# Performance work log

Measured on AMD Instinct MI355X. Metric: run time of the kernel, lower is better.

## Reference

```python
import jax, jax.numpy as jnp
import numpy as np


def setup_inputs() -> dict:
    key = jax.random.key(0)
    k1, k2 = jax.random.split(key)
    B, C, H, W = 32, 512, 32, 32
    NUM_ITEM = 2048
    x = jax.random.normal(k1, (B, C, H, W), dtype=jnp.float32)
    # original uses uniform(-stdv, stdv) with stdv = 1/sqrt(dim)
    stdv = 1.0 / np.sqrt(C)
    mempool = jax.random.uniform(k2, (NUM_ITEM, C), dtype=jnp.float32, minval=-stdv, maxval=stdv)
    return {"x": x, "mempool": mempool, "k": 8}


def reference(x, mempool, k):
    B, C, H, W = x.shape
    num_item = mempool.shape[0]
    # permute to channels-last and flatten spatial: [N, C]
    q = jnp.transpose(x, (0, 2, 3, 1)).reshape(-1, C)
    # gating scores: [N, num_item]
    att = q @ mempool.T
    vals, idx = jax.lax.top_k(att, k)            # [N, k]
    vals = jax.nn.softmax(vals, axis=1)
    # scatter top-k softmax weights into mostly-zero [N, num_item] matrix
    rows = jnp.arange(q.shape[0])[:, None]
    att_sparse = jnp.zeros_like(att).at[rows, idx].set(vals)
    # dense combine: [N, C]
    out = att_sparse @ mempool
    out = out.reshape(B, H, W, C)
    return jnp.transpose(out, (0, 3, 1, 2))
```

## Files before the change

kernel.cpp:

```cpp
#include <hip/hip_runtime.h>

typedef __attribute__((ext_vector_type(4))) float f32x4;
typedef __attribute__((ext_vector_type(8))) short short8;

#define C_    512
#define HW_   1024
#define M_    2048
#define TN    32
#define NTILE 8
#define NKC   16
#define NSTEP (NTILE * NKC)
#define NCAND 16
#define NEG_INF (-1e30f)

#define ATT_BASE   32768
#define ATT_STRIDE 264
#define ARENA_SIZE 49664
#define CV_BASE  32768
#define CI_BASE  36992
#define SEL_BASE 41216
#define RFV_BASE 43264
#define QS 260

__device__ __forceinline__ unsigned short f2bf(float f) {
    unsigned u = __builtin_bit_cast(unsigned, f);
    u += 0x7fffu + ((u >> 16) & 1u);
    return (unsigned short)(u >> 16);
}
__device__ __forceinline__ float bf2f(unsigned short s) {
    return __builtin_bit_cast(float, (unsigned)s << 16);
}

__global__ __launch_bounds__(256) void convk(const float* __restrict__ in,
                                             unsigned short* __restrict__ ob) {
    int gid = blockIdx.x * 256 + threadIdx.x;
    int m  = gid >> 6;
    int ug = gid & 63;
    const float4* p = (const float4*)(in + (size_t)m * C_ + ug * 8);
    float4 v0 = p[0], v1 = p[1];
    int4 o;
    o.x = (int)f2bf(v0.x) | ((int)f2bf(v0.y) << 16);
    o.y = (int)f2bf(v0.z) | ((int)f2bf(v0.w) << 16);
    o.z = (int)f2bf(v1.x) | ((int)f2bf(v1.y) << 16);
    o.w = (int)f2bf(v1.z) | ((int)f2bf(v1.w) << 16);
    int kc = ug >> 2, u = ug & 3;
    *(int4*)((char*)ob + (size_t)kc * 131072 + m * 64 + (u << 4)) = o;
}

__global__ __launch_bounds__(256, 3) void memk(const float* __restrict__ x,
                                               const float* __restrict__ mempool,
                                               const unsigned short* __restrict__ membR,
                                               float* __restrict__ out) {
    __shared__ __align__(16) char arena[ARENA_SIZE];
    unsigned short* att16 = (unsigned short*)(arena + ATT_BASE);
    float* candv  = (float*)(arena + CV_BASE);
    int*   candi  = (int*)(arena + CI_BASE);
    int*   selidx = (int*)(arena + SEL_BASE);
    float* refv   = (float*)(arena + RFV_BASE);
    float* qs     = (float*)arena;
    float* w_lds  = (float*)(arena + 8192);
    int*   i_lds  = (int*)(arena + 9216);

    const int t   = threadIdx.x;
    const int l   = t & 63;
    const int w   = t >> 6;
    const int hi  = l >> 4;
    const int l15 = l & 15;
    const int n0  = blockIdx.x * TN;
    const int b   = n0 >> 10;
    const int hw0 = n0 & 1023;
    const float* xb = x + (size_t)b * C_ * HW_ + hw0;

    {
        const int row = t & 31, g = t >> 5;
        const float* xp = xb + row;
        char* Arow = arena + row * 1024;
        const int swz = (row & 7) << 4;
#pragma unroll 8
        for (int j = 0; j < 32; ++j) {
            int c = g * 64 + 2 * j;
            float f0 = xp[(size_t)c * HW_];
            float f1 = xp[(size_t)(c + 1) * HW_];
            unsigned pk = (unsigned)f2bf(f0) | ((unsigned)f2bf(f1) << 16);
            *(unsigned*)(Arow + ((2 * c) ^ swz)) = pk;
        }
    }
    __syncthreads();

    const int srow = t >> 2, stq = t & 3;
    float sv[8]; int si[8];
#pragma unroll
    for (int p = 0; p < 8; ++p) { sv[p] = NEG_INF; si[p] = 0x7fffffff; }

    const int aswz = (l15 & 7) << 4;
    const char* Ab0 = arena + l15 * 1024;
    const char* Ab1 = arena + (16 + l15) * 1024;
    const int hio = hi << 4;
    const char* bbase = (const char*)membR + w * 4096 + l15 * 64 + hi * 16;

    short8 bq[4], bp[4];
    {
        const char* p0 = bbase;
        const char* p1 = bbase + 131072;
#pragma unroll
        for (int itf = 0; itf < 4; ++itf) {
            bq[itf] = *(const short8*)(p0 + itf * 1024);
            bp[itf] = *(const short8*)(p1 + itf * 1024);
        }
    }

    for (int tile = 0; tile < NTILE; ++tile) {
        f32x4 acc[2][4];
#pragma unroll
        for (int rf = 0; rf < 2; ++rf)
#pragma unroll
            for (int itf = 0; itf < 4; ++itf) acc[rf][itf] = (f32x4)0.f;

#pragma unroll 4
        for (int kc = 0; kc < NKC; ++kc) {
            int s = tile * NKC + kc + 2;
            int sc = (s < NSTEP) ? s : 0;
            const char* pn = bbase + (size_t)(sc & 15) * 131072 + (size_t)(sc >> 4) * 16384;
            short8 bn[4];
#pragma unroll
            for (int itf = 0; itf < 4; ++itf) bn[itf] = *(const short8*)(pn + itf * 1024);

            const int ao = (kc * 64 + hio) ^ aswz;
            short8 a0 = *(const short8*)(Ab0 + ao);
            short8 a1 = *(const short8*)(Ab1 + ao);
#pragma unroll
            for (int itf = 0; itf < 4; ++itf) {
                acc[0][itf] = __builtin_amdgcn_mfma_f32_16x16x32_bf16(a0, bq[itf], acc[0][itf], 0, 0, 0);
                acc[1][itf] = __builtin_amdgcn_mfma_f32_16x16x32_bf16(a1, bq[itf], acc[1][itf], 0, 0, 0);
            }
#pragma unroll
            for (int itf = 0; itf < 4; ++itf) { bq[itf] = bp[itf]; bp[itf] = bn[itf]; }
        }

#pragma unroll
        for (int rf = 0; rf < 2; ++rf)
#pragma unroll
            for (int itf = 0; itf < 4; ++itf) {
                int col = w * 64 + itf * 16 + l15;
#pragma unroll
                for (int reg = 0; reg < 4; ++reg)
                    att16[(rf * 16 + hi * 4 + reg) * ATT_STRIDE + col] = f2bf(acc[rf][itf][reg]);
            }
        __syncthreads();

        const int m0 = tile * 256;
        if (t < 128) {
            const unsigned short* arow = att16 + srow * ATT_STRIDE;
#pragma unroll
            for (int v = 0; v < 8; ++v) {
                short8 pv = *(const short8*)(arow + stq * 8 + v * 32);
                float f[8];
#pragma unroll
                for (int e = 0; e < 8; ++e) f[e] = bf2f((unsigned short)pv[e]);
                float m01 = fmaxf(f[0], f[1]), m23 = fmaxf(f[2], f[3]);
                float m45 = fmaxf(f[4], f[5]), m67 = fmaxf(f[6], f[7]);
                float vmax = fmaxf(fmaxf(m01, m23), fmaxf(m45, m67));
                if (vmax > sv[0]) {
#pragma unroll
                    for (int e = 0; e < 8; ++e) {
                        if (f[e] > sv[0]) {
                            sv[0] = f[e]; si[0] = m0 + stq * 8 + v * 32 + e;
#pragma unroll
                            for (int p = 0; p < 7; ++p) {
                                if (sv[p] > sv[p + 1]) {
                                    float tv = sv[p]; sv[p] = sv[p + 1]; sv[p + 1] = tv;
                                    int   ti = si[p]; si[p] = si[p + 1]; si[p + 1] = ti;
                                }
                            }
                        }
                    }
                }
            }
        }
        __syncthreads();
    }

    if (t < 128) {
#pragma unroll
        for (int p = 0; p < 8; ++p) {
            candv[srow * 33 + stq * 8 + p] = sv[p];
            candi[srow * 33 + stq * 8 + p] = si[p];
        }
    }
    __syncthreads();

    if (t < TN) {
        const int row = t;
        int pos[4] = {7, 7, 7, 7};
        for (int s = 0; s < NCAND; ++s) {
            float vb = NEG_INF; int ib = 0x7fffffff; int qb = 0;
#pragma unroll
            for (int q = 0; q < 4; ++q) {
                if (pos[q] >= 0) {
                    float v = candv[row * 33 + q * 8 + pos[q]];
                    int  ii = candi[row * 33 + q * 8 + pos[q]];
                    if (v > vb || (v == vb && ii < ib)) { vb = v; ib = ii; qb = q; }
                }
            }
            selidx[row * NCAND + s] = ib;
#pragma unroll
            for (int q = 0; q < 4; ++q) if (q == qb) --pos[q];
        }
    }
    __syncthreads();

    int cnd[2];
    cnd[0] = selidx[t];
    cnd[1] = selidx[t + 256];
    float racc[2] = {0.f, 0.f};
#pragma unroll
    for (int ch = 0; ch < 2; ++ch) {
        const int c0 = ch * 256;
        __syncthreads();
        {
            const int r = t & 31, g = t >> 5;
            const float* xp = xb + r;
#pragma unroll 2
            for (int j = 0; j < 8; ++j) {
                int c = g * 32 + j * 4;
                f32x4 v;
                v[0] = xp[(size_t)(c0 + c + 0) * HW_];
                v[1] = xp[(size_t)(c0 + c + 1) * HW_];
                v[2] = xp[(size_t)(c0 + c + 2) * HW_];
                v[3] = xp[(size_t)(c0 + c + 3) * HW_];
                *(f32x4*)&qs[r * QS + c] = v;
            }
        }
        __syncthreads();
#pragma unroll
        for (int pp = 0; pp < 2; ++pp) {
            const int row = (t + 256 * pp) >> 4;
            const float4* mp = (const float4*)(mempool + (size_t)cnd[pp] * C_ + c0);
            const f32x4* qrow = (const f32x4*)&qs[row * QS];
            float a = racc[pp];
#pragma unroll 8
            for (int u = 0; u < 64; ++u) {
                f32x4 q4 = qrow[u];
                float4 m4 = mp[u];
                a = fmaf(q4[0], m4.x, a);
                a = fmaf(q4[1], m4.y, a);
                a = fmaf(q4[2], m4.z, a);
                a = fmaf(q4[3], m4.w, a);
            }
            racc[pp] = a;
        }
    }
    refv[t] = racc[0];
    refv[t + 256] = racc[1];
    __syncthreads();

    if (t < TN) {
        const int row = t;
        float rv[16]; int ri[16];
#pragma unroll
        for (int s = 0; s < 16; ++s) { rv[s] = refv[row * 16 + s]; ri[s] = selidx[row * 16 + s]; }
        float wv8[8]; int wi8[8];
#pragma unroll
        for (int sel = 0; sel < 8; ++sel) {
            float vb = NEG_INF; int ib = 0x7fffffff; int sb = 0;
            for (int s = 0; s < 16; ++s) {
                if (rv[s] > vb || (rv[s] == vb && ri[s] < ib)) { vb = rv[s]; ib = ri[s]; sb = s; }
            }
            rv[sb] = NEG_INF;
            wv8[sel] = vb; wi8[sel] = ib;
        }
        const float mx = wv8[0];
        float e[8]; float sum = 0.f;
#pragma unroll
        for (int j = 0; j < 8; ++j) { e[j] = expf(wv8[j] - mx); sum += e[j]; }
        const float inv = 1.f / sum;
#pragma unroll
        for (int j = 0; j < 8; ++j) { w_lds[row * 8 + j] = e[j] * inv; i_lds[row * 8 + j] = wi8[j]; }
    }
    __syncthreads();

    const int crow = t & 31;
    const int cw   = t >> 5;
    float wreg[8]; int ireg[8];
#pragma unroll
    for (int j = 0; j < 8; ++j) { wreg[j] = w_lds[crow * 8 + j]; ireg[j] = i_lds[crow * 8 + j]; }
    float* outb = out + (size_t)b * C_ * HW_ + hw0 + crow;
#pragma unroll 2
    for (int cg = 0; cg < 16; ++cg) {
        const int c = cw * 64 + cg * 4;
        float o0 = 0.f, o1 = 0.f, o2 = 0.f, o3 = 0.f;
#pragma unroll
        for (int j = 0; j < 8; ++j) {
            const float4 mp4 = *(const float4*)&mempool[(size_t)ireg[j] * C_ + c];
            o0 = fmaf(wreg[j], mp4.x, o0);
            o1 = fmaf(wreg[j], mp4.y, o1);
            o2 = fmaf(wreg[j], mp4.z, o2);
            o3 = fmaf(wreg[j], mp4.w, o3);
        }
        outb[(size_t)(c + 0) * HW_] = o0;
        outb[(size_t)(c + 1) * HW_] = o1;
        outb[(size_t)(c + 2) * HW_] = o2;
        outb[(size_t)(c + 3) * HW_] = o3;
    }
}

extern "C" void kernel_launch(void* const* d_in, const int* in_sizes, int n_in,
                              void* d_out, int out_size, void* d_ws, size_t ws_size,
                              hipStream_t stream) {
    const float* x       = (const float*)d_in[0];
    const float* mempool = (const float*)d_in[1];
    unsigned short* membR = (unsigned short*)d_ws;
    float* o = (float*)d_out;
    convk<<<dim3(512), dim3(256), 0, stream>>>(mempool, membR);
    memk<<<dim3(1024), dim3(256), 0, stream>>>(x, mempool, membR, o);
}
```

Before: 444.0 us.

## Double-buffer score tiles to overlap top-k scan with MFMA and prefetch refinement

Scores are now staged in two alternating LDS buffers, so the top-k scan of the previous tile runs alongside the next tile's GEMM. This removes one barrier per tile. The B-operand register prefetch is deepened from two steps to three, and the second x channel-half load for the fp32 refinement is issued before the first half's dot products. The cost is a larger LDS arena and occupancy lowered from 3 to 2 blocks per CU, plus more live registers.

```diff
diff --git a/kernel.cpp b/kernel.cpp
--- a/kernel.cpp
+++ b/kernel.cpp
@@ -9,17 +9,19 @@
 #define TN    32
 #define NTILE 8
 #define NKC   16
-#define NSTEP (NTILE * NKC)
 #define NCAND 16
 #define NEG_INF (-1e30f)
 
-#define ATT_BASE   32768
 #define ATT_STRIDE 264
-#define ARENA_SIZE 49664
+#define BUF0 32768
+#define BUF1 49664
+#define ARENA_SIZE 66560
 #define CV_BASE  32768
 #define CI_BASE  36992
 #define SEL_BASE 41216
 #define RFV_BASE 43264
+#define WL_BASE  45312
+#define IL_BASE  46336
 #define QS 260
 
 __device__ __forceinline__ unsigned short f2bf(float f) {
@@ -47,19 +49,49 @@
     *(int4*)((char*)ob + (size_t)kc * 131072 + m * 64 + (u << 4)) = o;
 }
 
-__global__ __launch_bounds__(256, 3) void memk(const float* __restrict__ x,
+__device__ __forceinline__ void scan_tile(const unsigned short* arow, int m0,
+                                          float* sv, int* si, int stq) {
+#pragma unroll
+    for (int v = 0; v < 8; ++v) {
+        short8 pv = *(const short8*)(arow + stq * 8 + v * 32);
+        float f[8];
+#pragma unroll
+        for (int e = 0; e < 8; ++e) f[e] = bf2f((unsigned short)pv[e]);
+        float m01 = fmaxf(f[0], f[1]), m23 = fmaxf(f[2], f[3]);
+        float m45 = fmaxf(f[4], f[5]), m67 = fmaxf(f[6], f[7]);
+        float vmax = fmaxf(fmaxf(m01, m23), fmaxf(m45, m67));
+        if (vmax > sv[0]) {
+#pragma unroll
+            for (int e = 0; e < 8; ++e) {
+                if (f[e] > sv[0]) {
+                    sv[0] = f[e]; si[0] = m0 + stq * 8 + v * 32 + e;
+#pragma unroll
+                    for (int p = 0; p < 7; ++p) {
+                        if (sv[p] > sv[p + 1]) {
+                            float tv = sv[p]; sv[p] = sv[p + 1]; sv[p + 1] = tv;
+                            int   ti = si[p]; si[p] = si[p + 1]; si[p + 1] = ti;
+                        }
+                    }
+                }
+            }
+        }
+    }
+}
+
+__global__ __launch_bounds__(256, 2) void memk(const float* __restrict__ x,
                                                const float* __restrict__ mempool,
                                                const unsigned short* __restrict__ membR,
                                                float* __restrict__ out) {
     __shared__ __align__(16) char arena[ARENA_SIZE];
-    unsigned short* att16 = (unsigned short*)(arena + ATT_BASE);
+    unsigned short* att0 = (unsigned short*)(arena + BUF0);
+    unsigned short* att1 = (unsigned short*)(arena + BUF1);
     float* candv  = (float*)(arena + CV_BASE);
     int*   candi  = (int*)(arena + CI_BASE);
     int*   selidx = (int*)(arena + SEL_BASE);
     float* refv   = (float*)(arena + RFV_BASE);
     float* qs     = (float*)arena;
-    float* w_lds  = (float*)(arena + 8192);
-    int*   i_lds  = (int*)(arena + 9216);
+    float* w_lds  = (float*)(arena + WL_BASE);
+    int*   i_lds  = (int*)(arena + IL_BASE);
 
     const int t   = threadIdx.x;
     const int l   = t & 63;
@@ -98,18 +130,18 @@
     const int hio = hi << 4;
     const char* bbase = (const char*)membR + w * 4096 + l15 * 64 + hi * 16;
 
-    short8 bq[4], bp[4];
-    {
-        const char* p0 = bbase;
-        const char* p1 = bbase + 131072;
-#pragma unroll
-        for (int itf = 0; itf < 4; ++itf) {
-            bq[itf] = *(const short8*)(p0 + itf * 1024);
-            bp[itf] = *(const short8*)(p1 + itf * 1024);
-        }
+    short8 bq[4], b1[4], b2[4];
+#pragma unroll
+    for (int itf = 0; itf < 4; ++itf) {
+        bq[itf] = *(const short8*)(bbase + itf * 1024);
+        b1[itf] = *(const short8*)(bbase + 131072 + itf * 1024);
+        b2[itf] = *(const short8*)(bbase + 262144 + itf * 1024);
     }
 
     for (int tile = 0; tile < NTILE; ++tile) {
+        unsigned short* dumpBuf = (tile & 1) ? att1 : att0;
+        unsigned short* scanBuf = (tile & 1) ? att0 : att1;
+
         f32x4 acc[2][4];
 #pragma unroll
         for (int rf = 0; rf < 2; ++rf)
@@ -118,9 +150,9 @@
 
 #pragma unroll 4
         for (int kc = 0; kc < NKC; ++kc) {
-            int s = tile * NKC + kc + 2;
-            int sc = (s < NSTEP) ? s : 0;
-            const char* pn = bbase + (size_t)(sc & 15) * 131072 + (size_t)(sc >> 4) * 16384;
+            int s3 = tile * NKC + kc + 3;
+            if (s3 > 127) s3 = 127;
+            const char* pn = bbase + (size_t)(s3 & 15) * 131072 + (size_t)(s3 >> 4) * 16384;
             short8 bn[4];
 #pragma unroll
             for (int itf = 0; itf < 4; ++itf) bn[itf] = *(const short8*)(pn + itf * 1024);
@@ -134,7 +166,7 @@
                 acc[1][itf] = __builtin_amdgcn_mfma_f32_16x16x32_bf16(a1, bq[itf], acc[1][itf], 0, 0, 0);
             }
 #pragma unroll
-            for (int itf = 0; itf < 4; ++itf) { bq[itf] = bp[itf]; bp[itf] = bn[itf]; }
+            for (int itf = 0; itf < 4; ++itf) { bq[itf] = b1[itf]; b1[itf] = b2[itf]; b2[itf] = bn[itf]; }
         }
 
 #pragma unroll
@@ -144,41 +176,16 @@
                 int col = w * 64 + itf * 16 + l15;
 #pragma unroll
                 for (int reg = 0; reg < 4; ++reg)
-                    att16[(rf * 16 + hi * 4 + reg) * ATT_STRIDE + col] = f2bf(acc[rf][itf][reg]);
-            }
+                    dumpBuf[(rf * 16 + hi * 4 + reg) * ATT_STRIDE + col] = f2bf(acc[rf][itf][reg]);
+            }
+
+        if (tile > 0 && t < 128)
+            scan_tile(scanBuf + srow * ATT_STRIDE, (tile - 1) * 256, sv, si, stq);
+
         __syncthreads();
-
-        const int m0 = tile * 256;
-        if (t < 128) {
-            const unsigned short* arow = att16 + srow * ATT_STRIDE;
-#pragma unroll
-            for (int v = 0; v < 8; ++v) {
-                short8 pv = *(const short8*)(arow + stq * 8 + v * 32);
-                float f[8];
-#pragma unroll
-                for (int e = 0; e < 8; ++e) f[e] = bf2f((unsigned short)pv[e]);
-                float m01 = fmaxf(f[0], f[1]), m23 = fmaxf(f[2], f[3]);
-                float m45 = fmaxf(f[4], f[5]), m67 = fmaxf(f[6], f[7]);
-                float vmax = fmaxf(fmaxf(m01, m23), fmaxf(m45, m67));
-                if (vmax > sv[0]) {
-#pragma unroll
-                    for (int e = 0; e < 8; ++e) {
-                        if (f[e] > sv[0]) {
-                            sv[0] = f[e]; si[0] = m0 + stq * 8 + v * 32 + e;
-#pragma unroll
-                            for (int p = 0; p < 7; ++p) {
-                                if (sv[p] > sv[p + 1]) {
-                                    float tv = sv[p]; sv[p] = sv[p + 1]; sv[p + 1] = tv;
-                                    int   ti = si[p]; si[p] = si[p + 1]; si[p + 1] = ti;
-                                }
-                            }
-                        }
-                    }
-                }
-            }
-        }
-        __syncthreads();
-    }
+    }
+    if (t < 128)
+        scan_tile(att1 + srow * ATT_STRIDE, 7 * 256, sv, si, stq);
 
     if (t < 128) {
 #pragma unroll
@@ -213,42 +220,68 @@
     cnd[0] = selidx[t];
     cnd[1] = selidx[t + 256];
     float racc[2] = {0.f, 0.f};
-#pragma unroll
-    for (int ch = 0; ch < 2; ++ch) {
-        const int c0 = ch * 256;
-        __syncthreads();
-        {
-            const int r = t & 31, g = t >> 5;
-            const float* xp = xb + r;
+    const int qr = t & 31, qg = t >> 5;
+    const float* xq = xb + qr;
+
+    f32x4 r0[8];
 #pragma unroll 2
-            for (int j = 0; j < 8; ++j) {
-                int c = g * 32 + j * 4;
-                f32x4 v;
-                v[0] = xp[(size_t)(c0 + c + 0) * HW_];
-                v[1] = xp[(size_t)(c0 + c + 1) * HW_];
-                v[2] = xp[(size_t)(c0 + c + 2) * HW_];
-                v[3] = xp[(size_t)(c0 + c + 3) * HW_];
-                *(f32x4*)&qs[r * QS + c] = v;
-            }
-        }
-        __syncthreads();
-#pragma unroll
-        for (int pp = 0; pp < 2; ++pp) {
-            const int row = (t + 256 * pp) >> 4;
-            const float4* mp = (const float4*)(mempool + (size_t)cnd[pp] * C_ + c0);
-            const f32x4* qrow = (const f32x4*)&qs[row * QS];
-            float a = racc[pp];
+    for (int j = 0; j < 8; ++j) {
+        int c = qg * 32 + j * 4;
+        r0[j][0] = xq[(size_t)(c + 0) * HW_];
+        r0[j][1] = xq[(size_t)(c + 1) * HW_];
+        r0[j][2] = xq[(size_t)(c + 2) * HW_];
+        r0[j][3] = xq[(size_t)(c + 3) * HW_];
+    }
+#pragma unroll
+    for (int j = 0; j < 8; ++j) *(f32x4*)&qs[qr * QS + qg * 32 + j * 4] = r0[j];
+    __syncthreads();
+
+    f32x4 r1[8];
+#pragma unroll 2
+    for (int j = 0; j < 8; ++j) {
+        int c = 256 + qg * 32 + j * 4;
+        r1[j][0] = xq[(size_t)(c + 0) * HW_];
+        r1[j][1] = xq[(size_t)(c + 1) * HW_];
+        r1[j][2] = xq[(size_t)(c + 2) * HW_];
+        r1[j][3] = xq[(size_t)(c + 3) * HW_];
+    }
+#pragma unroll
+    for (int pp = 0; pp < 2; ++pp) {
+        const int row = (t + 256 * pp) >> 4;
+        const float4* mp = (const float4*)(mempool + (size_t)cnd[pp] * C_);
+        const f32x4* qrow = (const f32x4*)&qs[row * QS];
+        float a = racc[pp];
 #pragma unroll 8
-            for (int u = 0; u < 64; ++u) {
-                f32x4 q4 = qrow[u];
-                float4 m4 = mp[u];
-                a = fmaf(q4[0], m4.x, a);
-                a = fmaf(q4[1], m4.y, a);
-                a = fmaf(q4[2], m4.z, a);
-                a = fmaf(q4[3], m4.w, a);
-            }
-            racc[pp] = a;
-        }
+        for (int u = 0; u < 64; ++u) {
+            f32x4 q4 = qrow[u];
+            float4 m4 = mp[u];
+            a = fmaf(q4[0], m4.x, a);
+            a = fmaf(q4[1], m4.y, a);
+            a = fmaf(q4[2], m4.z, a);
+            a = fmaf(q4[3], m4.w, a);
+        }
+        racc[pp] = a;
+    }
+    __syncthreads();
+#pragma unroll
+    for (int j = 0; j < 8; ++j) *(f32x4*)&qs[qr * QS + qg * 32 + j * 4] = r1[j];
+    __syncthreads();
+#pragma unroll
+    for (int pp = 0; pp < 2; ++pp) {
+        const int row = (t + 256 * pp) >> 4;
+        const float4* mp = (const float4*)(mempool + (size_t)cnd[pp] * C_ + 256);
+        const f32x4* qrow = (const f32x4*)&qs[row * QS];
+        float a = racc[pp];
+#pragma unroll 8
+        for (int u = 0; u < 64; ++u) {
+            f32x4 q4 = qrow[u];
+            float4 m4 = mp[u];
+            a = fmaf(q4[0], m4.x, a);
+            a = fmaf(q4[1], m4.y, a);
+            a = fmaf(q4[2], m4.z, a);
+            a = fmaf(q4[3], m4.w, a);
+        }
+        racc[pp] = a;
     }
     refv[t] = racc[0];
     refv[t + 256] = racc[1];
```

Measured after the change: 462.6 us. 1.04x slower.

## Split fused kernel into tiled GEMM with per-tile top-8 and separate merge kernel

Applied to the files above, without the earlier changes.

Replaces the monolithic per-32-row kernel with a 2D-tiled GEMM kernel (128 rows x 128 items per block) that streams double-buffered bf16 activations through LDS, computes per-tile top-8 candidates, and writes packed value/index words to workspace. A second kernel merges the 16 per-tile candidate lists, then keeps the existing fp32 rescoring, softmax and combine. The aim is better B-operand reuse and parallelism across item tiles for the GEMM. The cost is an extra launch, a global round-trip for candidates, and repeated conversion of x across the 16 column tiles.

```diff
diff --git a/kernel.cpp b/kernel.cpp
--- a/kernel.cpp
+++ b/kernel.cpp
@@ -6,21 +6,7 @@
 #define C_    512
 #define HW_   1024
 #define M_    2048
-#define TN    32
-#define NTILE 8
-#define NKC   16
-#define NSTEP (NTILE * NKC)
-#define NCAND 16
 #define NEG_INF (-1e30f)
-
-#define ATT_BASE   32768
-#define ATT_STRIDE 264
-#define ARENA_SIZE 49664
-#define CV_BASE  32768
-#define CI_BASE  36992
-#define SEL_BASE 41216
-#define RFV_BASE 43264
-#define QS 260
 
 __device__ __forceinline__ unsigned short f2bf(float f) {
     unsigned u = __builtin_bit_cast(unsigned, f);
@@ -29,6 +15,20 @@
 }
 __device__ __forceinline__ float bf2f(unsigned short s) {
     return __builtin_bit_cast(float, (unsigned)s << 16);
+}
+__device__ __forceinline__ float pkval(unsigned u) {
+    return __builtin_bit_cast(float, u & 0xFFFF0000u);
+}
+
+__device__ __forceinline__ void insert8(float v, int idx, float* sv, int* si) {
+    sv[0] = v; si[0] = idx;
+#pragma unroll
+    for (int p = 0; p < 7; ++p) {
+        if (sv[p] > sv[p + 1]) {
+            float tv = sv[p]; sv[p] = sv[p + 1]; sv[p + 1] = tv;
+            int   ti = si[p]; si[p] = si[p + 1]; si[p + 1] = ti;
+        }
+    }
 }
 
 __global__ __launch_bounds__(256) void convk(const float* __restrict__ in,
@@ -47,140 +47,198 @@
     *(int4*)((char*)ob + (size_t)kc * 131072 + m * 64 + (u << 4)) = o;
 }
 
-__global__ __launch_bounds__(256, 3) void memk(const float* __restrict__ x,
-                                               const float* __restrict__ mempool,
-                                               const unsigned short* __restrict__ membR,
-                                               float* __restrict__ out) {
-    __shared__ __align__(16) char arena[ARENA_SIZE];
-    unsigned short* att16 = (unsigned short*)(arena + ATT_BASE);
-    float* candv  = (float*)(arena + CV_BASE);
-    int*   candi  = (int*)(arena + CI_BASE);
-    int*   selidx = (int*)(arena + SEL_BASE);
-    float* refv   = (float*)(arena + RFV_BASE);
-    float* qs     = (float*)arena;
-    float* w_lds  = (float*)(arena + 8192);
-    int*   i_lds  = (int*)(arena + 9216);
+#define K2_ABUF  9216
+#define K2_CAND  33792
+#define K2_ARENA 41984
+
+__global__ __launch_bounds__(256, 2) void gemmk(const float* __restrict__ x,
+                                                const unsigned short* __restrict__ membR,
+                                                unsigned int* __restrict__ gcand) {
+    __shared__ __align__(16) char arena[K2_ARENA];
+    unsigned short* att16 = (unsigned short*)arena;
+    unsigned int*   candt = (unsigned int*)(arena + K2_CAND);
 
     const int t   = threadIdx.x;
     const int l   = t & 63;
     const int w   = t >> 6;
     const int hi  = l >> 4;
     const int l15 = l & 15;
-    const int n0  = blockIdx.x * TN;
+    const int colTile = blockIdx.x;
+    const int rowTile = blockIdx.y;
+    const int n0  = rowTile * 128;
     const int b   = n0 >> 10;
     const int hw0 = n0 & 1023;
     const float* xb = x + (size_t)b * C_ * HW_ + hw0;
 
+    const char* bbase = (const char*)membR + colTile * 8192 + l15 * 64 + hi * 16;
+
+    short8 bq[8], bn[8];
+#pragma unroll
+    for (int itf = 0; itf < 8; ++itf) bq[itf] = *(const short8*)(bbase + itf * 1024);
+
     {
-        const int row = t & 31, g = t >> 5;
-        const float* xp = xb + row;
-        char* Arow = arena + row * 1024;
-        const int swz = (row & 7) << 4;
-#pragma unroll 8
-        for (int j = 0; j < 32; ++j) {
-            int c = g * 64 + 2 * j;
-            float f0 = xp[(size_t)c * HW_];
-            float f1 = xp[(size_t)(c + 1) * HW_];
-            unsigned pk = (unsigned)f2bf(f0) | ((unsigned)f2bf(f1) << 16);
-            *(unsigned*)(Arow + ((2 * c) ^ swz)) = pk;
-        }
-    }
-    __syncthreads();
+        char* buf = arena;
+#pragma unroll
+        for (int cc = 0; cc < 8; cc += 2) {
+            int c = w * 8 + cc;
+#pragma unroll
+            for (int rr = 0; rr < 2; ++rr) {
+                int row = rr * 64 + l;
+                float f0 = xb[(size_t)c * HW_ + row];
+                float f1 = xb[(size_t)(c + 1) * HW_ + row];
+                unsigned pk = (unsigned)f2bf(f0) | ((unsigned)f2bf(f1) << 16);
+                *(unsigned*)(buf + row * 72 + c * 2) = pk;
+            }
+        }
+    }
+    __syncthreads();
+
+    f32x4 acc[2][8];
+#pragma unroll
+    for (int rf = 0; rf < 2; ++rf)
+#pragma unroll
+        for (int itf = 0; itf < 8; ++itf) acc[rf][itf] = (f32x4)0.f;
+
+#pragma unroll 2
+    for (int kc = 0; kc < 16; ++kc) {
+        if (kc < 15) {
+            char* buf = arena + ((kc + 1) & 1) * K2_ABUF;
+            const float* xc = xb + (size_t)(kc + 1) * 32 * HW_;
+#pragma unroll
+            for (int cc = 0; cc < 8; cc += 2) {
+                int c = w * 8 + cc;
+#pragma unroll
+                for (int rr = 0; rr < 2; ++rr) {
+                    int row = rr * 64 + l;
+                    float f0 = xc[(size_t)c * HW_ + row];
+                    float f1 = xc[(size_t)(c + 1) * HW_ + row];
+                    unsigned pk = (unsigned)f2bf(f0) | ((unsigned)f2bf(f1) << 16);
+                    *(unsigned*)(buf + row * 72 + c * 2) = pk;
+                }
+            }
+        }
+        {
+            int s = (kc + 1 < 16) ? kc + 1 : 15;
+            const char* pn = bbase + (size_t)s * 131072;
+#pragma unroll
+            for (int itf = 0; itf < 8; ++itf) bn[itf] = *(const short8*)(pn + itf * 1024);
+        }
+        const char* cur = arena + (kc & 1) * K2_ABUF;
+        short8 a0 = *(const short8*)(cur + (w * 32 + l15) * 72 + hi * 16);
+        short8 a1 = *(const short8*)(cur + (w * 32 + 16 + l15) * 72 + hi * 16);
+#pragma unroll
+        for (int itf = 0; itf < 8; ++itf) {
+            acc[0][itf] = __builtin_amdgcn_mfma_f32_16x16x32_bf16(a0, bq[itf], acc[0][itf], 0, 0, 0);
+            acc[1][itf] = __builtin_amdgcn_mfma_f32_16x16x32_bf16(a1, bq[itf], acc[1][itf], 0, 0, 0);
+        }
+#pragma unroll
+        for (int itf = 0; itf < 8; ++itf) bq[itf] = bn[itf];
+        __syncthreads();
+    }
+
+#pragma unroll
+    for (int rf = 0; rf < 2; ++rf)
+#pragma unroll
+        for (int itf = 0; itf < 8; ++itf) {
+            int col = itf * 16 + l15;
+#pragma unroll
+            for (int reg = 0; reg < 4; ++reg) {
+                int row = w * 32 + rf * 16 + hi * 4 + reg;
+                att16[row * 132 + col] = f2bf(acc[rf][itf][reg]);
+            }
+        }
+    __syncthreads();
+
+    const int sr = t >> 1, hf = t & 1;
+    float sv[8]; int si[8];
+#pragma unroll
+    for (int p = 0; p < 8; ++p) { sv[p] = NEG_INF; si[p] = 0x7fffffff; }
+    {
+        const unsigned short* arow = att16 + sr * 132 + hf * 64;
+#pragma unroll
+        for (int v = 0; v < 8; ++v) {
+            short8 pv = *(const short8*)(arow + v * 8);
+            float f[8];
+#pragma unroll
+            for (int e = 0; e < 8; ++e) f[e] = bf2f((unsigned short)pv[e]);
+            float m01 = fmaxf(f[0], f[1]), m23 = fmaxf(f[2], f[3]);
+            float m45 = fmaxf(f[4], f[5]), m67 = fmaxf(f[6], f[7]);
+            float vmax = fmaxf(fmaxf(m01, m23), fmaxf(m45, m67));
+            if (vmax > sv[0]) {
+#pragma unroll
+                for (int e = 0; e < 8; ++e)
+                    if (f[e] > sv[0]) insert8(f[e], hf * 64 + v * 8 + e, sv, si);
+            }
+        }
+    }
+    __syncthreads();
+#pragma unroll
+    for (int p = 0; p < 8; ++p)
+        candt[(sr * 2 + hf) * 8 + p] =
+            (__builtin_bit_cast(unsigned, sv[p]) & 0xFFFF0000u) |
+            (unsigned)(colTile * 128 + si[p]);
+    __syncthreads();
+
+    if (t < 128) {
+        const unsigned* c0 = candt + (t * 2 + 0) * 8;
+        const unsigned* c1 = candt + (t * 2 + 1) * 8;
+        int p0 = 7, p1 = 7;
+        unsigned res[8];
+#pragma unroll
+        for (int s = 0; s < 8; ++s) {
+            unsigned u0 = c0[p0 < 0 ? 0 : p0], u1 = c1[p1 < 0 ? 0 : p1];
+            float v0 = (p0 >= 0) ? pkval(u0) : NEG_INF;
+            float v1 = (p1 >= 0) ? pkval(u1) : NEG_INF;
+            bool take0 = (v0 > v1) || (v0 == v1 && (int)(u0 & 0xFFFFu) < (int)(u1 & 0xFFFFu));
+            if (p1 < 0) take0 = true;
+            if (p0 < 0) take0 = false;
+            if (take0) { res[s] = u0; --p0; } else { res[s] = u1; --p1; }
+        }
+        unsigned int* gp = gcand + (size_t)(n0 + t) * 128 + colTile * 8;
+        *(uint4*)gp       = make_uint4(res[0], res[1], res[2], res[3]);
+        *(uint4*)(gp + 4) = make_uint4(res[4], res[5], res[6], res[7]);
+    }
+}
+
+#define QS 260
+#define K3_SEL 33280
+#define K3_RFV 35328
+#define K3_WL  37376
+#define K3_IL  38400
+#define K3_ARENA 39424
+#define NCAND 16
+
+__global__ __launch_bounds__(256, 4) void mergek(const float* __restrict__ x,
+                                                 const float* __restrict__ mempool,
+                                                 const unsigned int* __restrict__ gcand,
+                                                 float* __restrict__ out) {
+    __shared__ __align__(16) char arena[K3_ARENA];
+    float* candv  = (float*)arena;
+    int*   candi  = (int*)(arena + 4224);
+    float* qs     = (float*)arena;
+    int*   selidx = (int*)(arena + K3_SEL);
+    float* refv   = (float*)(arena + K3_RFV);
+    float* w_lds  = (float*)(arena + K3_WL);
+    int*   i_lds  = (int*)(arena + K3_IL);
+
+    const int t   = threadIdx.x;
+    const int n0  = blockIdx.x * 32;
+    const int b   = n0 >> 10;
+    const int hw0 = n0 & 1023;
+    const float* xb = x + (size_t)b * C_ * HW_ + hw0;
 
     const int srow = t >> 2, stq = t & 3;
     float sv[8]; int si[8];
 #pragma unroll
     for (int p = 0; p < 8; ++p) { sv[p] = NEG_INF; si[p] = 0x7fffffff; }
-
-    const int aswz = (l15 & 7) << 4;
-    const char* Ab0 = arena + l15 * 1024;
-    const char* Ab1 = arena + (16 + l15) * 1024;
-    const int hio = hi << 4;
-    const char* bbase = (const char*)membR + w * 4096 + l15 * 64 + hi * 16;
-
-    short8 bq[4], bp[4];
-    {
-        const char* p0 = bbase;
-        const char* p1 = bbase + 131072;
-#pragma unroll
-        for (int itf = 0; itf < 4; ++itf) {
-            bq[itf] = *(const short8*)(p0 + itf * 1024);
-            bp[itf] = *(const short8*)(p1 + itf * 1024);
-        }
-    }
-
-    for (int tile = 0; tile < NTILE; ++tile) {
-        f32x4 acc[2][4];
-#pragma unroll
-        for (int rf = 0; rf < 2; ++rf)
-#pragma unroll
-            for (int itf = 0; itf < 4; ++itf) acc[rf][itf] = (f32x4)0.f;
-
+    if (t < 128) {
+        const unsigned int* gc = gcand + (size_t)(n0 + srow) * 128 + stq * 32;
 #pragma unroll 4
-        for (int kc = 0; kc < NKC; ++kc) {
-            int s = tile * NKC + kc + 2;
-            int sc = (s < NSTEP) ? s : 0;
-            const char* pn = bbase + (size_t)(sc & 15) * 131072 + (size_t)(sc >> 4) * 16384;
-            short8 bn[4];
-#pragma unroll
-            for (int itf = 0; itf < 4; ++itf) bn[itf] = *(const short8*)(pn + itf * 1024);
-
-            const int ao = (kc * 64 + hio) ^ aswz;
-            short8 a0 = *(const short8*)(Ab0 + ao);
-            short8 a1 = *(const short8*)(Ab1 + ao);
-#pragma unroll
-            for (int itf = 0; itf < 4; ++itf) {
-                acc[0][itf] = __builtin_amdgcn_mfma_f32_16x16x32_bf16(a0, bq[itf], acc[0][itf], 0, 0, 0);
-                acc[1][itf] = __builtin_amdgcn_mfma_f32_16x16x32_bf16(a1, bq[itf], acc[1][itf], 0, 0, 0);
-            }
-#pragma unroll
-            for (int itf = 0; itf < 4; ++itf) { bq[itf] = bp[itf]; bp[itf] = bn[itf]; }
-        }
-
-#pragma unroll
-        for (int rf = 0; rf < 2; ++rf)
-#pragma unroll
-            for (int itf = 0; itf < 4; ++itf) {
-                int col = w * 64 + itf * 16 + l15;
-#pragma unroll
-                for (int reg = 0; reg < 4; ++reg)
-                    att16[(rf * 16 + hi * 4 + reg) * ATT_STRIDE + col] = f2bf(acc[rf][itf][reg]);
-            }
-        __syncthreads();
-
-        const int m0 = tile * 256;
-        if (t < 128) {
-            const unsigned short* arow = att16 + srow * ATT_STRIDE;
-#pragma unroll
-            for (int v = 0; v < 8; ++v) {
-                short8 pv = *(const short8*)(arow + stq * 8 + v * 32);
-                float f[8];
-#pragma unroll
-                for (int e = 0; e < 8; ++e) f[e] = bf2f((unsigned short)pv[e]);
-                float m01 = fmaxf(f[0], f[1]), m23 = fmaxf(f[2], f[3]);
-                float m45 = fmaxf(f[4], f[5]), m67 = fmaxf(f[6], f[7]);
-                float vmax = fmaxf(fmaxf(m01, m23), fmaxf(m45, m67));
-                if (vmax > sv[0]) {
-#pragma unroll
-                    for (int e = 0; e < 8; ++e) {
-                        if (f[e] > sv[0]) {
-                            sv[0] = f[e]; si[0] = m0 + stq * 8 + v * 32 + e;
-#pragma unroll
-                            for (int p = 0; p < 7; ++p) {
-                                if (sv[p] > sv[p + 1]) {
-                                    float tv = sv[p]; sv[p] = sv[p + 1]; sv[p + 1] = tv;
-                                    int   ti = si[p]; si[p] = si[p + 1]; si[p + 1] = ti;
-                                }
-                            }
-                        }
-                    }
-                }
-            }
-        }
-        __syncthreads();
-    }
-
-    if (t < 128) {
+        for (int j = 0; j < 32; ++j) {
+            unsigned u = gc[j];
+            float v = pkval(u);
+            if (v > sv[0]) insert8(v, (int)(u & 0xFFFFu), sv, si);
+        }
 #pragma unroll
         for (int p = 0; p < 8; ++p) {
             candv[srow * 33 + stq * 8 + p] = sv[p];
@@ -189,7 +247,7 @@
     }
     __syncthreads();
 
-    if (t < TN) {
+    if (t < 32) {
         const int row = t;
         int pos[4] = {7, 7, 7, 7};
         for (int s = 0; s < NCAND; ++s) {
@@ -218,17 +276,17 @@
         const int c0 = ch * 256;
         __syncthreads();
         {
-            const int r = t & 31, g = t >> 5;
-            const float* xp = xb + r;
+            const int qr = t & 31, qg = t >> 5;
+            const float* xp = xb + qr;
 #pragma unroll 2
             for (int j = 0; j < 8; ++j) {
-                int c = g * 32 + j * 4;
+                int c = qg * 32 + j * 4;
                 f32x4 v;
                 v[0] = xp[(size_t)(c0 + c + 0) * HW_];
                 v[1] = xp[(size_t)(c0 + c + 1) * HW_];
                 v[2] = xp[(size_t)(c0 + c + 2) * HW_];
                 v[3] = xp[(size_t)(c0 + c + 3) * HW_];
-                *(f32x4*)&qs[r * QS + c] = v;
+                *(f32x4*)&qs[qr * QS + c] = v;
             }
         }
         __syncthreads();
@@ -254,7 +312,7 @@
     refv[t + 256] = racc[1];
     __syncthreads();
 
-    if (t < TN) {
+    if (t < 32) {
         const int row = t;
         float rv[16]; int ri[16];
 #pragma unroll
@@ -310,7 +368,9 @@
     const float* x       = (const float*)d_in[0];
     const float* mempool = (const float*)d_in[1];
     unsigned short* membR = (unsigned short*)d_ws;
+    unsigned int*   gcand = (unsigned int*)((char*)d_ws + (4u << 20));
     float* o = (float*)d_out;
     convk<<<dim3(512), dim3(256), 0, stream>>>(mempool, membR);
-    memk<<<dim3(1024), dim3(256), 0, stream>>>(x, mempool, membR, o);
-}
+    gemmk<<<dim3(16, 256), dim3(256), 0, stream>>>(x, membR, gcand);
+    mergek<<<dim3(1024), dim3(256), 0, stream>>>(x, mempool, gcand, o);
+}
```

New measurement: 492.7 us. +11.0%, slower.
